# Optimization experiments

Measured on AMD Instinct MI355X. Metric: run time of the kernel, lower is better.

The kernel has to match this reference:

```python
import jax, jax.numpy as jnp
import numpy as np

K_NEAREST = 5
EPS = 1e-6


def setup_inputs() -> dict:
    key = jax.random.key(0)
    k1, k2, k3 = jax.random.split(key, 3)
    N_Q, N_DB, D_OUT, D_AUX = 4096, 65536, 32, 32
    return {
        "embedding_features": jax.random.normal(k1, (N_Q, D_OUT), dtype=jnp.float32),
        "db_embedding": jax.random.normal(k2, (N_DB, D_OUT), dtype=jnp.float32),
        "auxiliary_features": jax.random.normal(k3, (N_DB, D_AUX), dtype=jnp.float32),
    }


def reference(embedding_features, db_embedding, auxiliary_features):
    d_out = embedding_features.shape[-1]
    q = embedding_features.reshape(-1, d_out)          # [Nq, D]
    db = db_embedding.reshape(-1, d_out)               # [Ndb, D]

    # Euclidean cdist via the expanded quadratic form (same math as torch.cdist p=2).
    q_sq = jnp.sum(q * q, axis=1, keepdims=True)       # [Nq, 1]
    db_sq = jnp.sum(db * db, axis=1)[None, :]          # [1, Ndb]
    dist_sq = q_sq + db_sq - 2.0 * (q @ db.T)          # [Nq, Ndb]
    distances = jnp.sqrt(jnp.maximum(dist_sq, 0.0))

    # k smallest distances == k largest of negated distances.
    neg_top, nearest_indices = jax.lax.top_k(-distances, K_NEAREST)  # [Nq, k]
    nearest_distances = -neg_top                                      # [Nq, k]

    aux = auxiliary_features.reshape(-1, auxiliary_features.shape[-1])
    nearest_aux = aux[nearest_indices]                 # [Nq, k, Daux]

    weights = 1.0 / (nearest_distances + EPS)
    weights = weights / jnp.sum(weights, axis=1, keepdims=True)

    return jnp.sum(nearest_aux * weights[..., None], axis=1)  # [Nq, Daux]
```

## Files before the change

### kernel.cpp

```cpp
#include <hip/hip_runtime.h>
#include <math.h>

#define N_Q   4096
#define N_DB  65536
#define DIM   32
#define KNN   5
#define NC    64
#define CH    (N_DB / NC)
#define TS    256
#define NSTG  (CH / TS)
#define NSUB  (TS / 32)
#define NCAND (NC * 6)
#define BIAS  256.0f

typedef _Float16 half8  __attribute__((ext_vector_type(8)));
typedef __fp16   fp16x2 __attribute__((ext_vector_type(2)));
typedef float floatx16  __attribute__((ext_vector_type(16)));

union H8  { half8 h; uint4 u4; unsigned u[4]; };
union F16 { floatx16 v; float4 q4[4]; float f[16]; unsigned w[16]; };
union HU  { fp16x2 h2; unsigned u; };

__device__ __forceinline__ unsigned cvt2(float a, float b) {
    HU t; t.h2 = __builtin_amdgcn_cvt_pkrtz(a, b);
    return t.u;
}

__global__ __launch_bounds__(512, 2) void k_scan(const float* __restrict__ Q,
                                                 const float* __restrict__ DB,
                                                 unsigned* __restrict__ cand) {
    __shared__ char  dbs[2][16384];
    __shared__ float hbs[2][TS];

    const int tid  = threadIdx.x;
    const int lane = tid & 63, w = tid >> 6;
    const int h = lane >> 5, qcol = lane & 31;
    const int chunk = blockIdx.x & (NC - 1);
    const int qb    = blockIdx.x >> 6;
    const int q     = qb * 256 + w * 32 + qcol;
    const int pbase = chunk * CH;

    const int spt = tid >> 1, shalf = tid & 1;
    const float* sgbase = DB + (size_t)(pbase + spt) * DIM + shalf * 16;

    float4 n0 = *(const float4*)(sgbase + 0);
    float4 n1 = *(const float4*)(sgbase + 4);
    float4 n2 = *(const float4*)(sgbase + 8);
    float4 n3 = *(const float4*)(sgbase + 12);

    const float* qp = Q + (size_t)q * DIM;
    float4 qa = *(const float4*)(qp + h * 8);
    float4 qb4 = *(const float4*)(qp + h * 8 + 4);
    float4 qc = *(const float4*)(qp + 16 + h * 8);
    float4 qd = *(const float4*)(qp + 16 + h * 8 + 4);
    H8 b1, b2;
    b1.u[0] = cvt2(qa.x, qa.y);  b1.u[1] = cvt2(qa.z, qa.w);
    b1.u[2] = cvt2(qb4.x, qb4.y); b1.u[3] = cvt2(qb4.z, qb4.w);
    b2.u[0] = cvt2(qc.x, qc.y);  b2.u[1] = cvt2(qc.z, qc.w);
    b2.u[2] = cvt2(qd.x, qd.y);  b2.u[3] = cvt2(qd.z, qd.w);

    auto stage_finish = [&](int buf, float4 f0, float4 f1, float4 f2, float4 f3) {
        float s = f0.x*f0.x + f0.y*f0.y + f0.z*f0.z + f0.w*f0.w
                + f1.x*f1.x + f1.y*f1.y + f1.z*f1.z + f1.w*f1.w
                + f2.x*f2.x + f2.y*f2.y + f2.z*f2.z + f2.w*f2.w
                + f3.x*f3.x + f3.y*f3.y + f3.z*f3.z + f3.w*f3.w;
        s += __shfl_xor(s, 1, 64);
        if (shalf == 0) hbs[buf][spt] = BIAS - 0.5f * s;
        uint4 ua, ub;
        ua.x = cvt2(f0.x, f0.y); ua.y = cvt2(f0.z, f0.w);
        ua.z = cvt2(f1.x, f1.y); ua.w = cvt2(f1.z, f1.w);
        ub.x = cvt2(f2.x, f2.y); ub.y = cvt2(f2.z, f2.w);
        ub.z = cvt2(f3.x, f3.y); ub.w = cvt2(f3.z, f3.w);
        char* base = dbs[buf] + (spt >> 5) * 2048 + (shalf * 2) * 512 + (spt & 31) * 16;
        *(uint4*)(base)       = ua;
        *(uint4*)(base + 512) = ub;
    };

    stage_finish(0, n0, n1, n2, n3);

    float tk[6];
#pragma unroll
    for (int r = 0; r < 6; ++r) tk[r] = 0.f;

    constexpr int ROWC[16] = {0,1,2,3, 8,9,10,11, 16,17,18,19, 24,25,26,27};

    for (int t = 0; t < NSTG; ++t) {
        __syncthreads();
        if (t + 1 < NSTG) {
            const float* g = sgbase + (size_t)(t + 1) * TS * DIM;
            n0 = *(const float4*)(g + 0);  n1 = *(const float4*)(g + 4);
            n2 = *(const float4*)(g + 8);  n3 = *(const float4*)(g + 12);
        }
        const int buf = t & 1;
        const char* base = dbs[buf];
#pragma unroll
        for (int sub = 0; sub < NSUB; ++sub) {
            const char* tb = base + sub * 2048;
            H8 a1, a2;
            a1.u4 = *(const uint4*)(tb + h * 512 + (lane & 31) * 16);
            a2.u4 = *(const uint4*)(tb + 1024 + h * 512 + (lane & 31) * 16);
            F16 c0;
            const float* hb = &hbs[buf][sub * 32 + 4 * h];
            c0.q4[0] = *(const float4*)(hb + 0);
            c0.q4[1] = *(const float4*)(hb + 8);
            c0.q4[2] = *(const float4*)(hb + 16);
            c0.q4[3] = *(const float4*)(hb + 24);
            floatx16 acc = __builtin_amdgcn_mfma_f32_32x32x16_f16(a1.h, b1.h, c0.v, 0, 0, 0);
            acc = __builtin_amdgcn_mfma_f32_32x32x16_f16(a2.h, b2.h, acc, 0, 0, 0);
            F16 pk; pk.v = acc;
            const unsigned meta = (unsigned)(((t * NSUB + sub) << 5) | (h << 2));
            float p[16];
#pragma unroll
            for (int r = 0; r < 16; ++r)
                p[r] = __uint_as_float((pk.w[r] & 0xFFFFFC00u) | meta | (unsigned)ROWC[r]);
            float hi[8], lo[8];
#pragma unroll
            for (int i = 0; i < 8; ++i) { hi[i] = fmaxf(p[2*i], p[2*i+1]); lo[i] = fminf(p[2*i], p[2*i+1]); }
            float H4[4], L4[4];
#pragma unroll
            for (int i = 0; i < 4; ++i) {
                H4[i] = fmaxf(hi[2*i], hi[2*i+1]);
                L4[i] = fmaxf(fmaxf(lo[2*i], lo[2*i+1]), fminf(hi[2*i], hi[2*i+1]));
            }
            float H2[2], L2[2];
#pragma unroll
            for (int i = 0; i < 2; ++i) {
                H2[i] = fmaxf(H4[2*i], H4[2*i+1]);
                L2[i] = fmaxf(fmaxf(L4[2*i], L4[2*i+1]), fminf(H4[2*i], H4[2*i+1]));
            }
            float c1 = fmaxf(H2[0], H2[1]);
            float c2 = fmaxf(fmaxf(L2[0], L2[1]), fminf(H2[0], H2[1]));
#pragma unroll
            for (int i = 0; i < 6; ++i) { float mx = fmaxf(tk[i], c1); c1 = fminf(tk[i], c1); tk[i] = mx; }
#pragma unroll
            for (int i = 1; i < 6; ++i) { float mx = fmaxf(tk[i], c2); c2 = fminf(tk[i], c2); tk[i] = mx; }
        }
        if (t + 1 < NSTG) stage_finish((t + 1) & 1, n0, n1, n2, n3);
    }

    float other[6];
#pragma unroll
    for (int i = 0; i < 6; ++i) other[i] = __shfl_xor(tk[i], 32, 64);
#pragma unroll
    for (int i = 0; i < 6; ++i) {
        float val = other[i];
#pragma unroll
        for (int j = 0; j < 6; ++j) { float mx = fmaxf(tk[j], val); val = fminf(tk[j], val); tk[j] = mx; }
    }
    if (h == 0) {
        unsigned* dst = cand + ((size_t)q * NC + chunk) * 6;
#pragma unroll
        for (int r = 0; r < 6; ++r) dst[r] = __float_as_uint(tk[r]);
    }
}

__global__ __launch_bounds__(256) void k_merge(const float* __restrict__ Q,
                                               const float* __restrict__ DB,
                                               const float* __restrict__ AUX,
                                               const unsigned* __restrict__ cand,
                                               float* __restrict__ out) {
    const int tid = threadIdx.x, lane = tid & 63, w = tid >> 6;
    const int q = blockIdx.x * 4 + w;

    const unsigned* cq = cand + (size_t)q * NCAND + (size_t)lane * 6;
    float cur[6];
#pragma unroll
    for (int r = 0; r < 6; ++r) cur[r] = __uint_as_float(cq[r]);

    float wv[12]; int wl[12];
#pragma unroll
    for (int r = 0; r < 12; ++r) {
        float bv = cur[0]; int bl = lane;
#pragma unroll
        for (int off = 32; off >= 1; off >>= 1) {
            float ov = __shfl_xor(bv, off, 64);
            int   ol = __shfl_xor(bl, off, 64);
            if (ov > bv || (ov == bv && ol < bl)) { bv = ov; bl = ol; }
        }
        wv[r] = bv; wl[r] = bl;
        if (bl == lane) {
#pragma unroll
            for (int s = 0; s < 5; ++s) cur[s] = cur[s + 1];
            cur[5] = -1.f;
        }
    }

    float dist = 1e30f; int dbi = 0x7fffffff;
    if (lane < 12) {
        unsigned u = __float_as_uint(wv[lane]) & 1023u;
        dbi = wl[lane] * CH + (int)u;
        const float4* dp = (const float4*)(DB + (size_t)dbi * DIM);
        const float4* qp = (const float4*)(Q + (size_t)q * DIM);
        float dot = 0.f, qs = 0.f, ds = 0.f;
#pragma unroll
        for (int j = 0; j < DIM / 4; ++j) {
            float4 a = qp[j], d = dp[j];
            dot += a.x * d.x + a.y * d.y + a.z * d.z + a.w * d.w;
            qs  += a.x * a.x + a.y * a.y + a.z * a.z + a.w * a.w;
            ds  += d.x * d.x + d.y * d.y + d.z * d.z + d.w * d.w;
        }
        dist = sqrtf(fmaxf(qs + ds - 2.f * dot, 0.f));
    }
    float wd[KNN]; int wi[KNN];
#pragma unroll
    for (int r = 0; r < KNN; ++r) {
        float bd = dist; int bi = dbi;
#pragma unroll
        for (int off = 32; off >= 1; off >>= 1) {
            float od = __shfl_xor(bd, off, 64);
            int   oi = __shfl_xor(bi, off, 64);
            if (od < bd || (od == bd && oi < bi)) { bd = od; bi = oi; }
        }
        wd[r] = bd; wi[r] = bi;
        if (dist == bd && dbi == bi) dist = 1e30f;
    }
    float ww[KNN], W = 0.f;
#pragma unroll
    for (int r = 0; r < KNN; ++r) { ww[r] = 1.f / (wd[r] + 1e-6f); W += ww[r]; }
    if (lane < DIM) {
        float o = 0.f;
#pragma unroll
        for (int r = 0; r < KNN; ++r) o += ww[r] * AUX[(size_t)wi[r] * DIM + lane];
        out[(size_t)q * DIM + lane] = o / W;
    }
}

extern "C" void kernel_launch(void* const* d_in, const int* in_sizes, int n_in,
                              void* d_out, int out_size, void* d_ws, size_t ws_size,
                              hipStream_t stream) {
    const float* Q   = (const float*)d_in[0];
    const float* DB  = (const float*)d_in[1];
    const float* AUX = (const float*)d_in[2];
    float* out = (float*)d_out;

    unsigned* cand = (unsigned*)d_ws;

    k_scan<<<(N_Q / 256) * NC, 512, 0, stream>>>(Q, DB, cand);
    k_merge<<<N_Q / 4, 256, 0, stream>>>(Q, DB, AUX, cand, out);
}
```

Baseline: 152.8 us.

## Pre-convert DB to fp16 once and stream tiles via global_load_lds

Adds a prep kernel that converts the database to fp16 in the MFMA-ready layout and precomputes the biased half-norms into workspace. The scan kernel then fills shared memory directly with global_load_lds DMA instead of loading fp32 into registers, converting, and storing to LDS every stage. It also shrinks blocks to 256 threads with 128 queries and a 128-point tile, and moves the h-bit tag out of the inner loop. The trade is an extra launch and a round trip of the fp16 copy through memory, plus twice as many blocks, each re-reading its DB chunk for fewer queries.

```diff
diff --git a/kernel.cpp b/kernel.cpp
--- a/kernel.cpp
+++ b/kernel.cpp
@@ -7,7 +7,7 @@
 #define KNN   5
 #define NC    64
 #define CH    (N_DB / NC)
-#define TS    256
+#define TS    128
 #define NSTG  (CH / TS)
 #define NSUB  (TS / 32)
 #define NCAND (NC * 6)
@@ -18,7 +18,7 @@
 typedef float floatx16  __attribute__((ext_vector_type(16)));
 
 union H8  { half8 h; uint4 u4; unsigned u[4]; };
-union F16 { floatx16 v; float4 q4[4]; float f[16]; unsigned w[16]; };
+union F16 { floatx16 v; float4 q4[4]; unsigned w[16]; };
 union HU  { fp16x2 h2; unsigned u; };
 
 __device__ __forceinline__ unsigned cvt2(float a, float b) {
@@ -26,27 +26,52 @@
     return t.u;
 }
 
-__global__ __launch_bounds__(512, 2) void k_scan(const float* __restrict__ Q,
-                                                 const float* __restrict__ DB,
+__device__ __forceinline__ void ld_lds16(const void* g, void* l) {
+    __builtin_amdgcn_global_load_lds((const __attribute__((address_space(1))) unsigned*)g,
+                                     (__attribute__((address_space(3))) unsigned*)l, 16, 0, 0);
+}
+__device__ __forceinline__ void ld_lds4(const void* g, void* l) {
+    __builtin_amdgcn_global_load_lds((const __attribute__((address_space(1))) unsigned*)g,
+                                     (__attribute__((address_space(3))) unsigned*)l, 4, 0, 0);
+}
+
+__global__ __launch_bounds__(256) void k_prep(const float* __restrict__ DB,
+                                              uint4* __restrict__ DBh,
+                                              float* __restrict__ hdb) {
+    int p = blockIdx.x * 256 + threadIdx.x;
+    const float4* src = (const float4*)(DB + (size_t)p * DIM);
+    float4 f[8]; float s = 0.f;
+#pragma unroll
+    for (int j = 0; j < 8; ++j) {
+        f[j] = src[j];
+        s += f[j].x * f[j].x + f[j].y * f[j].y + f[j].z * f[j].z + f[j].w * f[j].w;
+    }
+    hdb[p] = BIAS - 0.5f * s;
+    int t = p >> 5, r = p & 31;
+#pragma unroll
+    for (int gi = 0; gi < 4; ++gi) {
+        uint4 g;
+        g.x = cvt2(f[2 * gi].x, f[2 * gi].y);
+        g.y = cvt2(f[2 * gi].z, f[2 * gi].w);
+        g.z = cvt2(f[2 * gi + 1].x, f[2 * gi + 1].y);
+        g.w = cvt2(f[2 * gi + 1].z, f[2 * gi + 1].w);
+        DBh[(size_t)t * 128 + gi * 32 + r] = g;
+    }
+}
+
+__global__ __launch_bounds__(256, 4) void k_scan(const float* __restrict__ Q,
+                                                 const uint4* __restrict__ DBh,
+                                                 const float* __restrict__ hdb,
                                                  unsigned* __restrict__ cand) {
-    __shared__ char  dbs[2][16384];
+    __shared__ char  dbs[2][8192];
     __shared__ float hbs[2][TS];
 
-    const int tid  = threadIdx.x;
-    const int lane = tid & 63, w = tid >> 6;
+    const int tid = threadIdx.x, lane = tid & 63, w = tid >> 6;
     const int h = lane >> 5, qcol = lane & 31;
     const int chunk = blockIdx.x & (NC - 1);
     const int qb    = blockIdx.x >> 6;
-    const int q     = qb * 256 + w * 32 + qcol;
+    const int q     = qb * 128 + w * 32 + qcol;
     const int pbase = chunk * CH;
-
-    const int spt = tid >> 1, shalf = tid & 1;
-    const float* sgbase = DB + (size_t)(pbase + spt) * DIM + shalf * 16;
-
-    float4 n0 = *(const float4*)(sgbase + 0);
-    float4 n1 = *(const float4*)(sgbase + 4);
-    float4 n2 = *(const float4*)(sgbase + 8);
-    float4 n3 = *(const float4*)(sgbase + 12);
 
     const float* qp = Q + (size_t)q * DIM;
     float4 qa = *(const float4*)(qp + h * 8);
@@ -54,43 +79,35 @@
     float4 qc = *(const float4*)(qp + 16 + h * 8);
     float4 qd = *(const float4*)(qp + 16 + h * 8 + 4);
     H8 b1, b2;
-    b1.u[0] = cvt2(qa.x, qa.y);  b1.u[1] = cvt2(qa.z, qa.w);
+    b1.u[0] = cvt2(qa.x, qa.y);   b1.u[1] = cvt2(qa.z, qa.w);
     b1.u[2] = cvt2(qb4.x, qb4.y); b1.u[3] = cvt2(qb4.z, qb4.w);
-    b2.u[0] = cvt2(qc.x, qc.y);  b2.u[1] = cvt2(qc.z, qc.w);
-    b2.u[2] = cvt2(qd.x, qd.y);  b2.u[3] = cvt2(qd.z, qd.w);
-
-    auto stage_finish = [&](int buf, float4 f0, float4 f1, float4 f2, float4 f3) {
-        float s = f0.x*f0.x + f0.y*f0.y + f0.z*f0.z + f0.w*f0.w
-                + f1.x*f1.x + f1.y*f1.y + f1.z*f1.z + f1.w*f1.w
-                + f2.x*f2.x + f2.y*f2.y + f2.z*f2.z + f2.w*f2.w
-                + f3.x*f3.x + f3.y*f3.y + f3.z*f3.z + f3.w*f3.w;
-        s += __shfl_xor(s, 1, 64);
-        if (shalf == 0) hbs[buf][spt] = BIAS - 0.5f * s;
-        uint4 ua, ub;
-        ua.x = cvt2(f0.x, f0.y); ua.y = cvt2(f0.z, f0.w);
-        ua.z = cvt2(f1.x, f1.y); ua.w = cvt2(f1.z, f1.w);
-        ub.x = cvt2(f2.x, f2.y); ub.y = cvt2(f2.z, f2.w);
-        ub.z = cvt2(f3.x, f3.y); ub.w = cvt2(f3.z, f3.w);
-        char* base = dbs[buf] + (spt >> 5) * 2048 + (shalf * 2) * 512 + (spt & 31) * 16;
-        *(uint4*)(base)       = ua;
-        *(uint4*)(base + 512) = ub;
+    b2.u[0] = cvt2(qc.x, qc.y);   b2.u[1] = cvt2(qc.z, qc.w);
+    b2.u[2] = cvt2(qd.x, qd.y);   b2.u[3] = cvt2(qd.z, qd.w);
+
+    unsigned maskv;
+    asm("v_mov_b32 %0, 0xFFFFFC00" : "=v"(maskv));
+
+    auto stage = [&](int buf, int t) {
+        const char* s = (const char*)DBh + (size_t)pbase * 64 + (size_t)t * 8192
+                        + w * 1024 + lane * 16;
+        char* d = dbs[buf] + w * 1024;
+        ld_lds16(s, d);
+        ld_lds16(s + 4096, d + 4096);
+        if (w < 2)
+            ld_lds4(hdb + pbase + t * TS + w * 64 + lane,
+                    (char*)&hbs[buf][0] + w * 256);
     };
 
-    stage_finish(0, n0, n1, n2, n3);
-
     float tk[6];
 #pragma unroll
     for (int r = 0; r < 6; ++r) tk[r] = 0.f;
 
     constexpr int ROWC[16] = {0,1,2,3, 8,9,10,11, 16,17,18,19, 24,25,26,27};
 
+    stage(0, 0);
     for (int t = 0; t < NSTG; ++t) {
         __syncthreads();
-        if (t + 1 < NSTG) {
-            const float* g = sgbase + (size_t)(t + 1) * TS * DIM;
-            n0 = *(const float4*)(g + 0);  n1 = *(const float4*)(g + 4);
-            n2 = *(const float4*)(g + 8);  n3 = *(const float4*)(g + 12);
-        }
+        if (t + 1 < NSTG) stage((t + 1) & 1, t + 1);
         const int buf = t & 1;
         const char* base = dbs[buf];
 #pragma unroll
@@ -108,11 +125,11 @@
             floatx16 acc = __builtin_amdgcn_mfma_f32_32x32x16_f16(a1.h, b1.h, c0.v, 0, 0, 0);
             acc = __builtin_amdgcn_mfma_f32_32x32x16_f16(a2.h, b2.h, acc, 0, 0, 0);
             F16 pk; pk.v = acc;
-            const unsigned meta = (unsigned)(((t * NSUB + sub) << 5) | (h << 2));
+            const int meta = (t * NSUB + sub) << 5;
             float p[16];
 #pragma unroll
             for (int r = 0; r < 16; ++r)
-                p[r] = __uint_as_float((pk.w[r] & 0xFFFFFC00u) | meta | (unsigned)ROWC[r]);
+                p[r] = __uint_as_float((pk.w[r] & maskv) | (unsigned)(meta | ROWC[r]));
             float hi[8], lo[8];
 #pragma unroll
             for (int i = 0; i < 8; ++i) { hi[i] = fmaxf(p[2*i], p[2*i+1]); lo[i] = fminf(p[2*i], p[2*i+1]); }
@@ -135,8 +152,11 @@
 #pragma unroll
             for (int i = 1; i < 6; ++i) { float mx = fmaxf(tk[i], c2); c2 = fminf(tk[i], c2); tk[i] = mx; }
         }
-        if (t + 1 < NSTG) stage_finish((t + 1) & 1, n0, n1, n2, n3);
-    }
+    }
+
+#pragma unroll
+    for (int r = 0; r < 6; ++r)
+        tk[r] = __uint_as_float(__float_as_uint(tk[r]) | (unsigned)(h << 2));
 
     float other[6];
 #pragma unroll
@@ -233,8 +253,12 @@
     const float* AUX = (const float*)d_in[2];
     float* out = (float*)d_out;
 
-    unsigned* cand = (unsigned*)d_ws;
-
-    k_scan<<<(N_Q / 256) * NC, 512, 0, stream>>>(Q, DB, cand);
+    char* ws = (char*)d_ws;
+    uint4*    DBh = (uint4*)ws;                         ws += (size_t)(N_DB / 32) * 128 * 16;
+    float*    hdb = (float*)ws;                         ws += (size_t)N_DB * 4;
+    unsigned* cand = (unsigned*)ws;
+
+    k_prep<<<N_DB / 256, 256, 0, stream>>>(DB, DBh, hdb);
+    k_scan<<<(N_Q / 128) * NC, 256, 0, stream>>>(Q, DBh, hdb, cand);
     k_merge<<<N_Q / 4, 256, 0, stream>>>(Q, DB, AUX, cand, out);
 }
```

New measurement: 138.9 us. -9.1%, faster.
